# Kernel optimization log

Hardware: AMD Instinct MI355X
Metric: run time of the kernel (lower is better)

Reference implementation:

```python
import jax, jax.numpy as jnp
import numpy as np
import math

N, D, H = 4096, 2048, 16
HD = D // H  # head_dim = 128


def setup_inputs() -> dict:
    key = jax.random.key(0)
    ks = jax.random.split(key, 9)
    s = 1.0 / math.sqrt(D)
    return {
        "x":  jax.random.normal(ks[0], (N, D), dtype=jnp.float32),
        "Wq": jax.random.normal(ks[1], (D, D), dtype=jnp.float32) * s,
        "bq": jax.random.normal(ks[2], (D,), dtype=jnp.float32) * s,
        "Wk": jax.random.normal(ks[3], (D, D), dtype=jnp.float32) * s,
        "bk": jax.random.normal(ks[4], (D,), dtype=jnp.float32) * s,
        "Wv": jax.random.normal(ks[5], (D, D), dtype=jnp.float32) * s,
        "bv": jax.random.normal(ks[6], (D,), dtype=jnp.float32) * s,
        "Wo": jax.random.normal(ks[7], (D, D), dtype=jnp.float32) * s,
        "bo": jax.random.normal(ks[8], (D,), dtype=jnp.float32) * s,
    }


def reference(x, Wq, bq, Wk, bk, Wv, bv, Wo, bo):
    # eqx.nn.Linear: y = W @ x + b, weight shape (out, in) -> x @ W.T + b
    q = x @ Wq.T + bq            # [N, D]
    k = x @ Wk.T + bk            # [N, D]
    v = x @ Wv.T + bv            # [N, D]
    q = q.reshape(N, H, HD).transpose(1, 0, 2)   # [H, N, hd]
    k = k.reshape(N, H, HD).transpose(1, 2, 0)   # [H, hd, N]
    v = v.reshape(N, H, HD).transpose(1, 0, 2)   # [H, N, hd]
    scale = 1.0 / math.sqrt(HD)
    scores = jnp.matmul(q * scale, k)            # [H, N, N]
    attn = jax.nn.softmax(scores, axis=-1)
    ctx = jnp.matmul(attn, v)                    # [H, N, hd]
    ctx = ctx.transpose(1, 0, 2).reshape(N, D)   # [N, D]
    return ctx @ Wo.T + bo
```

## Files before the change

### kernel.cpp

```cpp
#include <hip/hip_runtime.h>
#include <stdint.h>

#define N_TOK 4096
#define DIM   2048
#define NH    16
#define HD    128
#define NW    (DIM * DIM)

using bf16x8 = __attribute__((ext_vector_type(8))) short;
using bf16x4 = __attribute__((ext_vector_type(4))) short;
using f32x4  = __attribute__((ext_vector_type(4))) float;
using u32x2  = __attribute__((ext_vector_type(2))) unsigned int;

#if __has_builtin(__builtin_amdgcn_exp2f)
#define EXP2(x) __builtin_amdgcn_exp2f(x)
#else
#define EXP2(x) exp2f(x)
#endif

__device__ inline unsigned short f2bf(float f) {
  union { float f; unsigned u; } v; v.f = f;
  unsigned r = v.u + 0x7FFFu + ((v.u >> 16) & 1u);
  return (unsigned short)(r >> 16);
}
__device__ inline float bf2f(unsigned short u) {
  union { unsigned u; float f; } v; v.u = ((unsigned)u) << 16; return v.f;
}
__device__ inline f32x4 mfma16(bf16x8 a, bf16x8 b, f32x4 c) {
  return __builtin_amdgcn_mfma_f32_16x16x32_bf16(a, b, c, 0, 0, 0);
}
__device__ inline void gll16(const unsigned short* g, unsigned short* l) {
  __builtin_amdgcn_global_load_lds(
      (const __attribute__((address_space(1))) void*)g,
      (__attribute__((address_space(3))) void*)l, 16, 0, 0);
}

__device__ inline unsigned cvtpk_bf16(float lo, float hi) {
  unsigned r;
  asm("v_cvt_pk_bf16_f32 %0, %1, %2" : "=v"(r) : "v"(lo), "v"(hi));
  return r;
}

__device__ inline u32x2 pl32swap(unsigned a, unsigned b) {
#if __has_builtin(__builtin_amdgcn_permlane32_swap)
  return __builtin_amdgcn_permlane32_swap(a, b, false, false);
#else
  int lane = threadIdx.x & 63;
  unsigned as = (unsigned)__shfl_xor((int)a, 32);
  unsigned bs = (unsigned)__shfl_xor((int)b, 32);
  u32x2 r;
  r.x = (lane & 32) ? bs : a;
  r.y = (lane & 32) ? b : as;
  return r;
#endif
}
__device__ inline u32x2 pl16swap(unsigned a, unsigned b) {
#if __has_builtin(__builtin_amdgcn_permlane16_swap)
  return __builtin_amdgcn_permlane16_swap(a, b, false, false);
#else
  int lane = threadIdx.x & 63;
  unsigned as = (unsigned)__shfl_xor((int)a, 16);
  unsigned bs = (unsigned)__shfl_xor((int)b, 16);
  u32x2 r;
  r.x = (lane & 16) ? bs : a;
  r.y = (lane & 16) ? b : as;
  return r;
#endif
}

__global__ __launch_bounds__(256)
void cvt_bf16(const float* __restrict__ src, unsigned short* __restrict__ dst, int n) {
  int i = blockIdx.x * 256 + threadIdx.x;
  if (i * 8 >= n) return;
  const float4* s = (const float4*)src + (size_t)i * 2;
  float4 a = s[0], b = s[1];
  bf16x8 o;
  o[0] = (short)f2bf(a.x); o[1] = (short)f2bf(a.y);
  o[2] = (short)f2bf(a.z); o[3] = (short)f2bf(a.w);
  o[4] = (short)f2bf(b.x); o[5] = (short)f2bf(b.y);
  o[6] = (short)f2bf(b.z); o[7] = (short)f2bf(b.w);
  *(bf16x8*)(dst + (size_t)i * 8) = o;
}

template<int OUT_MODE>
__global__ __launch_bounds__(256)
void gemm_bf16(const unsigned short* __restrict__ A, const unsigned short* __restrict__ B,
               const float* __restrict__ bias, void* __restrict__ out_, float scale) {
  __shared__ unsigned short Asl[128 * 32];
  __shared__ unsigned short Bsl[128 * 32];
  const int tid  = threadIdx.x;
  const int lane = tid & 63, w = tid >> 6;
  const int wy = w >> 1, wx = w & 1;
  const int lr = lane & 15, quad = lane >> 4;
  const int m0 = blockIdx.y * 128, n0 = blockIdx.x * 128;

  const f32x4 vzero = {0.f, 0.f, 0.f, 0.f};
  f32x4 acc[4][4];
#pragma unroll
  for (int i = 0; i < 4; ++i)
#pragma unroll
    for (int j = 0; j < 4; ++j) acc[i][j] = vzero;

  for (int k0 = 0; k0 < DIM; k0 += 32) {
    __syncthreads();
#pragma unroll
    for (int i = 0; i < 2; ++i) {
      int ch = tid + i * 256;
      int r = ch >> 2, cc = ch & 3;
      gll16(&A[(size_t)(m0 + r) * DIM + k0 + cc * 8], &Asl[ch * 8]);
      gll16(&B[(size_t)(n0 + r) * DIM + k0 + cc * 8], &Bsl[ch * 8]);
    }
    __syncthreads();

    bf16x8 af[4], bfv[4];
#pragma unroll
    for (int mb = 0; mb < 4; ++mb)
      af[mb] = *(const bf16x8*)&Asl[(wy * 64 + mb * 16 + lr) * 32 + quad * 8];
#pragma unroll
    for (int nb = 0; nb < 4; ++nb)
      bfv[nb] = *(const bf16x8*)&Bsl[(wx * 64 + nb * 16 + lr) * 32 + quad * 8];
#pragma unroll
    for (int mb = 0; mb < 4; ++mb)
#pragma unroll
      for (int nb = 0; nb < 4; ++nb)
        acc[mb][nb] = mfma16(af[mb], bfv[nb], acc[mb][nb]);
  }

#pragma unroll
  for (int mb = 0; mb < 4; ++mb)
#pragma unroll
    for (int nb = 0; nb < 4; ++nb) {
      int gn = n0 + wx * 64 + nb * 16 + lr;
      int gm_base = m0 + wy * 64 + mb * 16 + quad * 4;
      float bs = bias[gn];
      if constexpr (OUT_MODE == 2) {
        bf16x4 pk;
#pragma unroll
        for (int r = 0; r < 4; ++r) pk[r] = (short)f2bf((acc[mb][nb][r] + bs) * scale);
        *(bf16x4*)&((unsigned short*)out_)[(size_t)gn * N_TOK + gm_base] = pk;
      } else {
#pragma unroll
        for (int r = 0; r < 4; ++r) {
          float v = (acc[mb][nb][r] + bs) * scale;
          if constexpr (OUT_MODE == 1)
            ((float*)out_)[(size_t)(gm_base + r) * DIM + gn] = v;
          else
            ((unsigned short*)out_)[(size_t)(gm_base + r) * DIM + gn] = f2bf(v);
        }
      }
    }
}

__global__ __launch_bounds__(256, 1)
void flash_attn(const unsigned short* __restrict__ Q,
                const unsigned short* __restrict__ K,
                const unsigned short* __restrict__ Vt,
                unsigned short* __restrict__ ctx) {
  constexpr int LDK = 136;
  constexpr int LDV = 72;
  constexpr int NT  = N_TOK / 64;
  __shared__ unsigned short Ksl[64 * LDK];
  __shared__ unsigned short VTsl[128 * LDV];

  const int tid  = threadIdx.x;
  const int lane = tid & 63, w = tid >> 6;
  const int lr = lane & 15, quad = lane >> 4;
  const int hoff = blockIdx.y * HD;
  const int q0   = blockIdx.x * 256;
  const int qw   = q0 + w * 64;

  bf16x8 qf[4][4];
#pragma unroll
  for (int mb = 0; mb < 4; ++mb)
#pragma unroll
    for (int c = 0; c < 4; ++c)
      qf[mb][c] = *(const bf16x8*)&Q[(size_t)(qw + mb * 16 + lr) * DIM + hoff + c * 32 + quad * 8];

  const f32x4 vzero = {0.f, 0.f, 0.f, 0.f};
  f32x4 o[4][8];
  float l_acc[4] = {0.f, 0.f, 0.f, 0.f};
#pragma unroll
  for (int mb = 0; mb < 4; ++mb)
#pragma unroll
    for (int nb = 0; nb < 8; ++nb) o[mb][nb] = vzero;

  bf16x8 kreg[4], vreg[4];
  auto load_tile = [&](int kt) {
    int kbase = kt * 64;
#pragma unroll
    for (int i = 0; i < 4; ++i) {
      int ch = tid + i * 256;
      kreg[i] = *(const bf16x8*)&K[(size_t)(kbase + (ch >> 4)) * DIM + hoff + (ch & 15) * 8];
      vreg[i] = *(const bf16x8*)&Vt[(size_t)(hoff + (ch >> 3)) * N_TOK + kbase + (ch & 7) * 8];
    }
  };
  load_tile(0);

  for (int kt = 0; kt < NT; ++kt) {
    __syncthreads();
#pragma unroll
    for (int i = 0; i < 4; ++i) {
      int ch = tid + i * 256;
      *(bf16x8*)&Ksl[(ch >> 4) * LDK + (ch & 15) * 8] = kreg[i];
      *(bf16x8*)&VTsl[(ch >> 3) * LDV + (ch & 7) * 8] = vreg[i];
    }
    __syncthreads();
    if (kt + 1 < NT) load_tile(kt + 1);

    f32x4 s[4][4];
#pragma unroll
    for (int mb = 0; mb < 4; ++mb)
#pragma unroll
      for (int nf = 0; nf < 4; ++nf) s[mb][nf] = vzero;
#pragma unroll
    for (int nf = 0; nf < 4; ++nf)
#pragma unroll
      for (int c = 0; c < 4; ++c) {
        bf16x8 kf = *(const bf16x8*)&Ksl[(nf * 16 + lr) * LDK + c * 32 + quad * 8];
#pragma unroll
        for (int mb = 0; mb < 4; ++mb) s[mb][nf] = mfma16(kf, qf[mb][c], s[mb][nf]);
      }

    bf16x8 pf[4][2];
#pragma unroll
    for (int mb = 0; mb < 4; ++mb) {
      unsigned W[4][2];
      float lp = 0.f;
#pragma unroll
      for (int nf = 0; nf < 4; ++nf) {
        float e0 = EXP2(s[mb][nf][0]);
        float e1 = EXP2(s[mb][nf][1]);
        float e2 = EXP2(s[mb][nf][2]);
        float e3 = EXP2(s[mb][nf][3]);
        lp += (e0 + e1) + (e2 + e3);
        W[nf][0] = cvtpk_bf16(e0, e1);
        W[nf][1] = cvtpk_bf16(e2, e3);
      }
      l_acc[mb] += lp;
#pragma unroll
      for (int ki = 0; ki < 2; ++ki) {
        u32x2 a0  = pl32swap(W[2 * ki][0], W[2 * ki + 1][0]);
        u32x2 t02 = pl16swap(a0.x, a0.y);
        u32x2 a1  = pl32swap(W[2 * ki][1], W[2 * ki + 1][1]);
        u32x2 t13 = pl16swap(a1.x, a1.y);
        union { unsigned u[4]; bf16x8 v; } pu;
        pu.u[0] = t02.x; pu.u[1] = t13.x; pu.u[2] = t02.y; pu.u[3] = t13.y;
        pf[mb][ki] = pu.v;
      }
    }

#pragma unroll
    for (int nb = 0; nb < 8; ++nb)
#pragma unroll
      for (int ki = 0; ki < 2; ++ki) {
        bf16x8 vf = *(const bf16x8*)&VTsl[(nb * 16 + lr) * LDV + ki * 32 + quad * 8];
#pragma unroll
        for (int mb = 0; mb < 4; ++mb) o[mb][nb] = mfma16(pf[mb][ki], vf, o[mb][nb]);
      }
  }

#pragma unroll
  for (int mb = 0; mb < 4; ++mb) {
    float t = l_acc[mb];
    t += __shfl_xor(t, 16);
    t += __shfl_xor(t, 32);
    l_acc[mb] = t;
  }
#pragma unroll
  for (int mb = 0; mb < 4; ++mb)
#pragma unroll
    for (int r = 0; r < 4; ++r) {
      float Lr = __shfl(l_acc[mb], quad * 4 + r);
      float inv = 1.0f / Lr;
      int gq = qw + mb * 16 + quad * 4 + r;
#pragma unroll
      for (int nb = 0; nb < 8; ++nb)
        ctx[(size_t)gq * DIM + hoff + nb * 16 + lr] = f2bf(o[mb][nb][r] * inv);
    }
}

extern "C" void kernel_launch(void* const* d_in, const int* in_sizes, int n_in,
                              void* d_out, int out_size, void* d_ws, size_t ws_size,
                              hipStream_t stream) {
  (void)in_sizes; (void)n_in; (void)out_size; (void)ws_size;
  const float* x  = (const float*)d_in[0];
  const float* Wq = (const float*)d_in[1];
  const float* bq = (const float*)d_in[2];
  const float* Wk = (const float*)d_in[3];
  const float* bk = (const float*)d_in[4];
  const float* Wv = (const float*)d_in[5];
  const float* bv = (const float*)d_in[6];
  const float* Wo = (const float*)d_in[7];
  const float* bo = (const float*)d_in[8];

  const size_t NE = (size_t)N_TOK * DIM;
  unsigned short* xb  = (unsigned short*)d_ws;
  unsigned short* Wqb = xb + NE;
  unsigned short* Wkb = Wqb + NW;
  unsigned short* Wvb = Wkb + NW;
  unsigned short* Wob = Wvb + NW;
  unsigned short* Qb  = Wob + NW;
  unsigned short* Kb  = Qb + NE;
  unsigned short* Vtb = Kb + NE;

  cvt_bf16<<<4096, 256, 0, stream>>>(x,  xb,  (int)NE);
  cvt_bf16<<<2048, 256, 0, stream>>>(Wq, Wqb, NW);
  cvt_bf16<<<2048, 256, 0, stream>>>(Wk, Wkb, NW);
  cvt_bf16<<<2048, 256, 0, stream>>>(Wv, Wvb, NW);
  cvt_bf16<<<2048, 256, 0, stream>>>(Wo, Wob, NW);

  dim3 gemm_grid(DIM / 128, N_TOK / 128);
  const float qscale = 1.4426950408889634f * 0.08838834764831845f;

  gemm_bf16<0><<<gemm_grid, 256, 0, stream>>>(xb, Wqb, bq, Qb, qscale);
  gemm_bf16<0><<<gemm_grid, 256, 0, stream>>>(xb, Wkb, bk, Kb, 1.0f);
  gemm_bf16<2><<<gemm_grid, 256, 0, stream>>>(xb, Wvb, bv, Vtb, 1.0f);

  unsigned short* ctxb = xb;
  flash_attn<<<dim3(N_TOK / 256, NH), 256, 0, stream>>>(Qb, Kb, Vtb, ctxb);

  gemm_bf16<1><<<gemm_grid, 256, 0, stream>>>(ctxb, Wob, bo, (float*)d_out, 1.0f);
}
```

Before: 491.1 us.

## Fuse conversions and QKV GEMMs, double-buffer GEMM with swizzled LDS, remap grids

Merges the five fp32-to-bf16 conversion launches into one kernel and the three QKV projection GEMMs into one launch indexed by blockIdx. The GEMM core moves to BK=64 with double-buffered LDS, XOR-swizzled shared layout to avoid bank conflicts, prefetch of the next K tile overlapping MFMA, setprio around MFMA and occupancy hint of 2. Block indices are remapped for XCD/L2 locality in GEMMs and flash attention. Adds complexity with more barriers per iteration and larger LDS use.

```diff
diff --git a/kernel.cpp b/kernel.cpp
--- a/kernel.cpp
+++ b/kernel.cpp
@@ -33,6 +33,11 @@
   __builtin_amdgcn_global_load_lds(
       (const __attribute__((address_space(1))) void*)g,
       (__attribute__((address_space(3))) void*)l, 16, 0, 0);
+}
+__device__ inline void wgbar() {
+  asm volatile("" ::: "memory");
+  __builtin_amdgcn_s_barrier();
+  asm volatile("" ::: "memory");
 }
 
 __device__ inline unsigned cvtpk_bf16(float lo, float hi) {
@@ -69,85 +74,179 @@
 }
 
 __global__ __launch_bounds__(256)
-void cvt_bf16(const float* __restrict__ src, unsigned short* __restrict__ dst, int n) {
-  int i = blockIdx.x * 256 + threadIdx.x;
-  if (i * 8 >= n) return;
-  const float4* s = (const float4*)src + (size_t)i * 2;
+void cvt_all(const float* __restrict__ x,  const float* __restrict__ Wq,
+             const float* __restrict__ Wk, const float* __restrict__ Wv,
+             const float* __restrict__ Wo, unsigned short* __restrict__ dst) {
+  const int item = blockIdx.x * 256 + threadIdx.x;
+  constexpr int XI = 1 << 20;
+  constexpr int WI = 1 << 19;
+  const float* src;
+  if (item < XI) {
+    src = x + (size_t)item * 8;
+  } else {
+    int j = item - XI;
+    int m = j >> 19;
+    int jj = j & (WI - 1);
+    const float* Ws[4] = {Wq, Wk, Wv, Wo};
+    src = Ws[m] + (size_t)jj * 8;
+  }
+  const float4* s = (const float4*)src;
   float4 a = s[0], b = s[1];
   bf16x8 o;
   o[0] = (short)f2bf(a.x); o[1] = (short)f2bf(a.y);
   o[2] = (short)f2bf(a.z); o[3] = (short)f2bf(a.w);
   o[4] = (short)f2bf(b.x); o[5] = (short)f2bf(b.y);
   o[6] = (short)f2bf(b.z); o[7] = (short)f2bf(b.w);
-  *(bf16x8*)(dst + (size_t)i * 8) = o;
-}
-
-template<int OUT_MODE>
-__global__ __launch_bounds__(256)
-void gemm_bf16(const unsigned short* __restrict__ A, const unsigned short* __restrict__ B,
-               const float* __restrict__ bias, void* __restrict__ out_, float scale) {
-  __shared__ unsigned short Asl[128 * 32];
-  __shared__ unsigned short Bsl[128 * 32];
-  const int tid  = threadIdx.x;
-  const int lane = tid & 63, w = tid >> 6;
-  const int wy = w >> 1, wx = w & 1;
-  const int lr = lane & 15, quad = lane >> 4;
-  const int m0 = blockIdx.y * 128, n0 = blockIdx.x * 128;
-
-  const f32x4 vzero = {0.f, 0.f, 0.f, 0.f};
-  f32x4 acc[4][4];
-#pragma unroll
-  for (int i = 0; i < 4; ++i)
-#pragma unroll
-    for (int j = 0; j < 4; ++j) acc[i][j] = vzero;
-
-  for (int k0 = 0; k0 < DIM; k0 += 32) {
-    __syncthreads();
-#pragma unroll
-    for (int i = 0; i < 2; ++i) {
-      int ch = tid + i * 256;
-      int r = ch >> 2, cc = ch & 3;
-      gll16(&A[(size_t)(m0 + r) * DIM + k0 + cc * 8], &Asl[ch * 8]);
-      gll16(&B[(size_t)(n0 + r) * DIM + k0 + cc * 8], &Bsl[ch * 8]);
-    }
-    __syncthreads();
-
-    bf16x8 af[4], bfv[4];
-#pragma unroll
-    for (int mb = 0; mb < 4; ++mb)
-      af[mb] = *(const bf16x8*)&Asl[(wy * 64 + mb * 16 + lr) * 32 + quad * 8];
-#pragma unroll
-    for (int nb = 0; nb < 4; ++nb)
-      bfv[nb] = *(const bf16x8*)&Bsl[(wx * 64 + nb * 16 + lr) * 32 + quad * 8];
-#pragma unroll
-    for (int mb = 0; mb < 4; ++mb)
-#pragma unroll
-      for (int nb = 0; nb < 4; ++nb)
-        acc[mb][nb] = mfma16(af[mb], bfv[nb], acc[mb][nb]);
+  *(bf16x8*)(dst + (size_t)item * 8) = o;
+}
+
+#define GEMM_CORE(A_, B_, m0_, n0_)                                          \
+  constexpr int BM = 128, BN = 128, BK = 64;                                 \
+  constexpr int NKT = DIM / BK;                                              \
+  __shared__ unsigned short Asl[2][BM * BK];                                 \
+  __shared__ unsigned short Bsl[2][BN * BK];                                 \
+  const int tid  = threadIdx.x;                                              \
+  const int lane = tid & 63;                                                 \
+  const int w    = tid >> 6;                                                 \
+  const int wm = w >> 1, wn = w & 1;                                         \
+  const int lr = lane & 15, quad = lane >> 4;                                \
+  const f32x4 vzero = {0.f, 0.f, 0.f, 0.f};                                  \
+  f32x4 acc[4][4];                                                           \
+  _Pragma("unroll")                                                          \
+  for (int i = 0; i < 4; ++i)                                                \
+    _Pragma("unroll")                                                        \
+    for (int j = 0; j < 4; ++j) acc[i][j] = vzero;                           \
+  size_t asrc[4]; int aldst[4];                                              \
+  size_t bsrc[4]; int bldst[4];                                              \
+  _Pragma("unroll")                                                          \
+  for (int i = 0; i < 4; ++i) {                                              \
+    int ch = tid + i * 256;                                                  \
+    int row = ch >> 3, cc = ch & 7;                                          \
+    int gcc = cc ^ (row & 7);                                                \
+    asrc[i]  = (size_t)((m0_) + row) * DIM + gcc * 8;                        \
+    aldst[i] = ch * 8;                                                       \
+    bsrc[i]  = (size_t)((n0_) + row) * DIM + gcc * 8;                        \
+    bldst[i] = ch * 8;                                                       \
+  }                                                                          \
+  auto stage_all = [&](int buf, int k0) {                                    \
+    _Pragma("unroll")                                                        \
+    for (int i = 0; i < 4; ++i) gll16(&(A_)[asrc[i] + k0], &Asl[buf][aldst[i]]); \
+    _Pragma("unroll")                                                        \
+    for (int i = 0; i < 4; ++i) gll16(&(B_)[bsrc[i] + k0], &Bsl[buf][bldst[i]]); \
+  };                                                                         \
+  auto lda = [&](int buf, int ks, bf16x8* af) {                              \
+    _Pragma("unroll")                                                        \
+    for (int mb = 0; mb < 4; ++mb) {                                         \
+      int row  = wm * 64 + mb * 16 + lr;                                     \
+      int slot = (ks * 4 + quad) ^ (row & 7);                                \
+      af[mb] = *(const bf16x8*)&Asl[buf][row * 64 + slot * 8];               \
+    }                                                                        \
+  };                                                                         \
+  auto ldb = [&](int buf, int ks, bf16x8* bfv) {                             \
+    _Pragma("unroll")                                                        \
+    for (int nb2 = 0; nb2 < 4; ++nb2) {                                      \
+      int row  = wn * 64 + nb2 * 16 + lr;                                    \
+      int slot = (ks * 4 + quad) ^ (row & 7);                                \
+      bfv[nb2] = *(const bf16x8*)&Bsl[buf][row * 64 + slot * 8];             \
+    }                                                                        \
+  };                                                                         \
+  auto mm = [&](bf16x8* af, bf16x8* bfv) {                                   \
+    __builtin_amdgcn_s_setprio(1);                                           \
+    _Pragma("unroll")                                                        \
+    for (int mb = 0; mb < 4; ++mb)                                           \
+      _Pragma("unroll")                                                      \
+      for (int nb2 = 0; nb2 < 4; ++nb2)                                      \
+        acc[mb][nb2] = mfma16(af[mb], bfv[nb2], acc[mb][nb2]);               \
+    __builtin_amdgcn_s_setprio(0);                                           \
+  };                                                                         \
+  stage_all(0, 0);                                                           \
+  asm volatile("s_waitcnt vmcnt(0)" ::: "memory");                           \
+  wgbar();                                                                   \
+  for (int t = 0; t < NKT - 1; ++t) {                                        \
+    const int buf = t & 1, sk = (t + 1) * BK;                                \
+    bf16x8 af[4], bfv[4];                                                    \
+    lda(buf, 0, af); ldb(buf, 0, bfv);                                       \
+    stage_all(buf ^ 1, sk);                                                  \
+    wgbar();                                                                 \
+    mm(af, bfv);                                                             \
+    wgbar();                                                                 \
+    lda(buf, 1, af); ldb(buf, 1, bfv);                                       \
+    asm volatile("s_waitcnt vmcnt(0)" ::: "memory");                         \
+    wgbar();                                                                 \
+    mm(af, bfv);                                                             \
+    wgbar();                                                                 \
+  }                                                                          \
+  {                                                                          \
+    const int buf = (NKT - 1) & 1;                                           \
+    bf16x8 af[4], bfv[4];                                                    \
+    lda(buf, 0, af); ldb(buf, 0, bfv);                                       \
+    mm(af, bfv);                                                             \
+    lda(buf, 1, af); ldb(buf, 1, bfv);                                       \
+    mm(af, bfv);                                                             \
   }
 
+__global__ __launch_bounds__(256, 2)
+void gemm_qkv(const unsigned short* __restrict__ A,
+              const unsigned short* __restrict__ WqB,
+              const unsigned short* __restrict__ WkB,
+              const unsigned short* __restrict__ WvB,
+              const float* __restrict__ bq, const float* __restrict__ bk,
+              const float* __restrict__ bv,
+              unsigned short* __restrict__ Qout,
+              unsigned short* __restrict__ Kout,
+              unsigned short* __restrict__ Vtout, float qscale) {
+  const int z     = blockIdx.x >> 9;
+  const int inner = blockIdx.x & 511;
+  const int nb  = (inner & 7) * 64 + (inner >> 3);
+  const int m0  = (nb >> 4) * 128;
+  const int n0  = (nb & 15) * 128;
+  const unsigned short* B = (z == 0) ? WqB : (z == 1) ? WkB : WvB;
+  const float* bias       = (z == 0) ? bq  : (z == 1) ? bk  : bv;
+  const float scale       = (z == 0) ? qscale : 1.0f;
+
+  GEMM_CORE(A, B, m0, n0)
+
 #pragma unroll
   for (int mb = 0; mb < 4; ++mb)
 #pragma unroll
-    for (int nb = 0; nb < 4; ++nb) {
-      int gn = n0 + wx * 64 + nb * 16 + lr;
-      int gm_base = m0 + wy * 64 + mb * 16 + quad * 4;
+    for (int nb2 = 0; nb2 < 4; ++nb2) {
+      int gn = n0 + wn * 64 + nb2 * 16 + lr;
+      int gm_base = m0 + wm * 64 + mb * 16 + quad * 4;
       float bs = bias[gn];
-      if constexpr (OUT_MODE == 2) {
+      if (z == 2) {
         bf16x4 pk;
 #pragma unroll
-        for (int r = 0; r < 4; ++r) pk[r] = (short)f2bf((acc[mb][nb][r] + bs) * scale);
-        *(bf16x4*)&((unsigned short*)out_)[(size_t)gn * N_TOK + gm_base] = pk;
+        for (int r = 0; r < 4; ++r) pk[r] = (short)f2bf(acc[mb][nb2][r] + bs);
+        *(bf16x4*)&Vtout[(size_t)gn * N_TOK + gm_base] = pk;
       } else {
-#pragma unroll
-        for (int r = 0; r < 4; ++r) {
-          float v = (acc[mb][nb][r] + bs) * scale;
-          if constexpr (OUT_MODE == 1)
-            ((float*)out_)[(size_t)(gm_base + r) * DIM + gn] = v;
-          else
-            ((unsigned short*)out_)[(size_t)(gm_base + r) * DIM + gn] = f2bf(v);
-        }
+        unsigned short* out = (z == 0) ? Qout : Kout;
+#pragma unroll
+        for (int r = 0; r < 4; ++r)
+          out[(size_t)(gm_base + r) * DIM + gn] = f2bf((acc[mb][nb2][r] + bs) * scale);
       }
+    }
+}
+
+__global__ __launch_bounds__(256, 2)
+void gemm_out(const unsigned short* __restrict__ A, const unsigned short* __restrict__ B,
+              const float* __restrict__ bias, float* __restrict__ out_) {
+  const int bid = blockIdx.x;
+  const int nb  = (bid & 7) * 64 + (bid >> 3);
+  const int m0  = (nb >> 4) * 128;
+  const int n0  = (nb & 15) * 128;
+
+  GEMM_CORE(A, B, m0, n0)
+
+#pragma unroll
+  for (int mb = 0; mb < 4; ++mb)
+#pragma unroll
+    for (int nb2 = 0; nb2 < 4; ++nb2) {
+      int gn = n0 + wn * 64 + nb2 * 16 + lr;
+      int gm_base = m0 + wm * 64 + mb * 16 + quad * 4;
+      float bs = bias[gn];
+#pragma unroll
+      for (int r = 0; r < 4; ++r)
+        out_[(size_t)(gm_base + r) * DIM + gn] = acc[mb][nb2][r] + bs;
     }
 }
 
@@ -165,8 +264,12 @@
   const int tid  = threadIdx.x;
   const int lane = tid & 63, w = tid >> 6;
   const int lr = lane & 15, quad = lane >> 4;
-  const int hoff = blockIdx.y * HD;
-  const int q0   = blockIdx.x * 256;
+
+  const int bid  = blockIdx.x;
+  const int head = (bid & 7) * 2 + ((bid >> 3) & 1);
+  const int qblk = bid >> 4;
+  const int hoff = head * HD;
+  const int q0   = qblk * 256;
   const int qw   = q0 + w * 64;
 
   bf16x8 qf[4][4];
@@ -303,21 +406,15 @@
   unsigned short* Kb  = Qb + NE;
   unsigned short* Vtb = Kb + NE;
 
-  cvt_bf16<<<4096, 256, 0, stream>>>(x,  xb,  (int)NE);
-  cvt_bf16<<<2048, 256, 0, stream>>>(Wq, Wqb, NW);
-  cvt_bf16<<<2048, 256, 0, stream>>>(Wk, Wkb, NW);
-  cvt_bf16<<<2048, 256, 0, stream>>>(Wv, Wvb, NW);
-  cvt_bf16<<<2048, 256, 0, stream>>>(Wo, Wob, NW);
-
-  dim3 gemm_grid(DIM / 128, N_TOK / 128);
+  cvt_all<<<12288, 256, 0, stream>>>(x, Wq, Wk, Wv, Wo, xb);
+
   const float qscale = 1.4426950408889634f * 0.08838834764831845f;
 
-  gemm_bf16<0><<<gemm_grid, 256, 0, stream>>>(xb, Wqb, bq, Qb, qscale);
-  gemm_bf16<0><<<gemm_grid, 256, 0, stream>>>(xb, Wkb, bk, Kb, 1.0f);
-  gemm_bf16<2><<<gemm_grid, 256, 0, stream>>>(xb, Wvb, bv, Vtb, 1.0f);
+  gemm_qkv<<<1536, 256, 0, stream>>>(xb, Wqb, Wkb, Wvb, bq, bk, bv,
+                                     Qb, Kb, Vtb, qscale);
 
   unsigned short* ctxb = xb;
-  flash_attn<<<dim3(N_TOK / 256, NH), 256, 0, stream>>>(Qb, Kb, Vtb, ctxb);
-
-  gemm_bf16<1><<<gemm_grid, 256, 0, stream>>>(ctxb, Wob, bo, (float*)d_out, 1.0f);
-}
+  flash_attn<<<256, 256, 0, stream>>>(Qb, Kb, Vtb, ctxb);
+
+  gemm_out<<<512, 256, 0, stream>>>(ctxb, Wob, bo, (float*)d_out);
+}
```

Measured after the change: 439.8 us. 1.12x faster.
